# Performance work log

Measured on AMD Instinct MI355X. Metric: run time of the kernel, lower is better.

The kernel has to match this reference:

```python
import jax, jax.numpy as jnp
import numpy as np

B, T, U, QS, MS = 64, 2048, 512, 512, 512

def setup_inputs() -> dict:
    key = jax.random.key(0)
    k1, k2, k3, k4, k5 = jax.random.split(key, 5)
    query = jax.random.normal(k1, (B, QS), dtype=jnp.float32)
    keys = jax.random.normal(k2, (B, T, MS), dtype=jnp.float32)
    # torch nn.Linear weights: [out, in], no bias
    Wq = jax.random.normal(k3, (U, QS), dtype=jnp.float32) * (1.0 / np.sqrt(QS))
    Wm = jax.random.normal(k4, (U, MS), dtype=jnp.float32) * (1.0 / np.sqrt(MS))
    Wa = jax.random.normal(k5, (1, U), dtype=jnp.float32) * (1.0 / np.sqrt(U))
    return {"query": query, "keys": keys, "Wq": Wq, "Wm": Wm, "Wa": Wa}

def reference(query, keys, Wq, Wm, Wa):
    # processed_query: [B, U]
    pq = jnp.einsum('bq,uq->bu', query, Wq)
    # values: [B, T, U]
    vals = jnp.einsum('btm,um->btu', keys, Wm)
    # alignment score: [B, T]
    score = jnp.einsum('btu,u->bt', jnp.tanh(pq[:, None, :] + vals), Wa[0])
    weight = jax.nn.softmax(score, axis=-1)            # [B, T]
    total_context = jnp.einsum('bt,btm->bm', weight, keys)  # [B, MS]
    return (total_context, score)
```

## Files before the change

kernel.cpp:

```cpp
#include <hip/hip_runtime.h>
#include <cstdint>
#include <cstddef>

#define Bn 64
#define Tn 2048
#define Un 512
#define QSn 512
#define MSn 512
#define TCH 64
#define NCH 32
#define NKT 16

using f32x16 = __attribute__((ext_vector_type(16))) float;
using bf16x8 = __attribute__((ext_vector_type(8))) short;

__device__ __forceinline__ unsigned short f2bf(float x) {
    unsigned int u = __float_as_uint(x);
    u += 0x7FFFu + ((u >> 16) & 1u);
    return (unsigned short)(u >> 16);
}

__device__ __forceinline__ unsigned int pk2bf(float lo, float hi) {
    unsigned int r;
    asm("v_cvt_pk_bf16_f32 %0, %1, %2" : "=v"(r) : "v"(lo), "v"(hi));
    return r;
}

__device__ __forceinline__ bf16x8 cvt8(float4 a, float4 b) {
    union { unsigned int u[4]; bf16x8 v; } r;
    r.u[0] = pk2bf(a.x, a.y);
    r.u[1] = pk2bf(a.z, a.w);
    r.u[2] = pk2bf(b.x, b.y);
    r.u[3] = pk2bf(b.z, b.w);
    return r.v;
}

__device__ __forceinline__ float tanh_fast(float x) {
    float e = exp2f(x * 2.885390043258667f);
    return 1.f - 2.f * __builtin_amdgcn_rcpf(e + 1.f);
}

#define GLOAD(G, L) __builtin_amdgcn_global_load_lds( \
    (const __attribute__((address_space(1))) void*)(G), \
    (__attribute__((address_space(3))) void*)(L), 16, 0, 0)

__global__ __launch_bounds__(256) void cvt_kernel(const float* __restrict__ src,
                                                  unsigned short* __restrict__ dst) {
    int i = blockIdx.x * 256 + threadIdx.x;
    float4 v = *(const float4*)(src + (size_t)i * 4);
    ushort4 h = { f2bf(v.x), f2bf(v.y), f2bf(v.z), f2bf(v.w) };
    *(ushort4*)&dst[(size_t)i * 4] = h;
}

__global__ __launch_bounds__(128) void pq_kernel(const float* __restrict__ query,
                                                 const float* __restrict__ Wq,
                                                 float* __restrict__ pq) {
    __shared__ float ql[QSn];
    const int b = blockIdx.x;
    const int quad = blockIdx.y;
    const int tid = threadIdx.x;
    for (int i = tid; i < QSn; i += 128) ql[i] = query[(size_t)b * QSn + i];
    __syncthreads();
    const int u = quad * 128 + tid;
    const float* w = Wq + (size_t)u * QSn;
    float a0 = 0.f, a1 = 0.f;
    #pragma unroll 4
    for (int k = 0; k < QSn; k += 8) {
        float4 w0 = *(const float4*)(w + k);
        float4 w1 = *(const float4*)(w + k + 4);
        float4 q0 = *(const float4*)(ql + k);
        float4 q1 = *(const float4*)(ql + k + 4);
        a0 += w0.x * q0.x + w0.y * q0.y + w0.z * q0.z + w0.w * q0.w;
        a1 += w1.x * q1.x + w1.y * q1.y + w1.z * q1.z + w1.w * q1.w;
    }
    pq[(size_t)b * Un + u] = a0 + a1;
}

__global__ __launch_bounds__(512, 4) void fused_kernel(const float* __restrict__ keys,
                                                       const unsigned short* __restrict__ WmB,
                                                       const float* __restrict__ pq,
                                                       const float* __restrict__ Wa,
                                                       float* __restrict__ score_out,
                                                       float* __restrict__ pm,
                                                       float* __restrict__ pl,
                                                       float* __restrict__ pctx) {
    __shared__ __align__(16) unsigned short Ah[2][TCH * 32];
    __shared__ __align__(16) unsigned short Bh[2][512 * 32];
    __shared__ float sc_lds[8][TCH];
    __shared__ float stot[TCH];
    __shared__ float wexp[TCH];

    const int tid = threadIdx.x;
    const int lane = tid & 63;
    const int w = tid >> 6;
    const int lc = lane & 31;
    const int l5 = lane >> 5;
    const int b = blockIdx.y;
    const int chunk = blockIdx.x;
    const int t0 = chunk * TCH;

    const int ar = tid >> 2;
    const int akg = tid & 3;
    const int awof = (tid >> 3) * 64 +
                     ((((akg << 1) | (ar & 1)) ^ ((tid >> 3) & 7)) * 8);
    const float* gA = keys + ((size_t)b * Tn + t0 + ar) * MSn + akg * 8;

    const int bg = (lane & 7) ^ ((lane >> 3) & 7);
    const unsigned short* gBw = WmB +
        (size_t)(w * 64 + (((lane >> 3) << 1) | (bg & 1))) * MSn + (bg >> 1) * 8;

    f32x16 acc[2][2];
    #pragma unroll
    for (int mf = 0; mf < 2; ++mf)
        #pragma unroll
        for (int nf = 0; nf < 2; ++nf)
            #pragma unroll
            for (int r = 0; r < 16; ++r) acc[mf][nf][r] = 0.f;

    {
        char* bD = (char*)&Bh[0][0] + w * 4096;
        #pragma unroll
        for (int j = 0; j < 4; ++j)
            GLOAD(gBw + (size_t)j * 16 * MSn, bD + j * 1024);
        if (tid < 256) {
            float4 p0 = *(const float4*)(gA);
            float4 p1 = *(const float4*)(gA + 4);
            *(bf16x8*)&Ah[0][awof] = cvt8(p0, p1);
        }
    }

    #pragma unroll
    for (int kt = 0; kt < NKT; ++kt) {
        __syncthreads();

        float4 p0, p1;
        if (kt < NKT - 1 && tid < 256) {
            const float* g = gA + (kt + 1) * 32;
            p0 = *(const float4*)(g);
            p1 = *(const float4*)(g + 4);
        }

        {
            const unsigned short* lA = &Ah[kt & 1][0];
            const unsigned short* lB = &Bh[kt & 1][0];
            #pragma unroll
            for (int ks = 0; ks < 2; ++ks) {
                bf16x8 af[2], bfr[2];
                #pragma unroll
                for (int mf = 0; mf < 2; ++mf) {
                    int r = mf * 32 + lc;
                    int gp = (((ks * 2 + l5) << 1) | (r & 1)) ^ ((r >> 1) & 7);
                    af[mf] = *(const bf16x8*)&lA[(r >> 1) * 64 + gp * 8];
                }
                #pragma unroll
                for (int nf = 0; nf < 2; ++nf) {
                    int ru = w * 64 + nf * 32 + lc;
                    int gp = (((ks * 2 + l5) << 1) | (ru & 1)) ^ ((ru >> 1) & 7);
                    bfr[nf] = *(const bf16x8*)&Bh[kt & 1][(ru >> 1) * 64 + gp * 8];
                    (void)lB;
                }
                #pragma unroll
                for (int mf = 0; mf < 2; ++mf)
                    #pragma unroll
                    for (int nf = 0; nf < 2; ++nf)
                        acc[mf][nf] = __builtin_amdgcn_mfma_f32_32x32x16_bf16(
                            af[mf], bfr[nf], acc[mf][nf], 0, 0, 0);
            }
        }

        __syncthreads();

        if (kt < NKT - 1) {
            char* bD = (char*)&Bh[(kt + 1) & 1][0] + w * 4096;
            const unsigned short* gb = gBw + (kt + 1) * 32;
            #pragma unroll
            for (int j = 0; j < 4; ++j)
                GLOAD(gb + (size_t)j * 16 * MSn, bD + j * 1024);
            if (tid < 256)
                *(bf16x8*)&Ah[(kt + 1) & 1][awof] = cvt8(p0, p1);
        }
    }

    float pqv[2], wav[2];
    #pragma unroll
    for (int nf = 0; nf < 2; ++nf) {
        int u = w * 64 + nf * 32 + lc;
        pqv[nf] = pq[(size_t)b * Un + u];
        wav[nf] = Wa[u];
    }
    #pragma unroll
    for (int mf = 0; mf < 2; ++mf) {
        #pragma unroll
        for (int r = 0; r < 16; ++r) {
            float s = tanh_fast(acc[mf][0][r] + pqv[0]) * wav[0]
                    + tanh_fast(acc[mf][1][r] + pqv[1]) * wav[1];
            s += __shfl_xor(s, 16);
            s += __shfl_xor(s, 8);
            s += __shfl_xor(s, 4);
            s += __shfl_xor(s, 2);
            s += __shfl_xor(s, 1);
            if (lc == 0)
                sc_lds[w][mf * 32 + (r & 3) + 8 * (r >> 2) + 4 * l5] = s;
        }
    }
    __syncthreads();
    if (tid < TCH) {
        float v = ((sc_lds[0][tid] + sc_lds[1][tid]) + (sc_lds[2][tid] + sc_lds[3][tid]))
                + ((sc_lds[4][tid] + sc_lds[5][tid]) + (sc_lds[6][tid] + sc_lds[7][tid]));
        stot[tid] = v;
        score_out[(size_t)b * Tn + t0 + tid] = v;
    }
    __syncthreads();

    if (tid < 64) {
        float v = stot[tid];
        float mx = v;
        #pragma unroll
        for (int off = 32; off; off >>= 1) mx = fmaxf(mx, __shfl_xor(mx, off));
        float e = __expf(v - mx);
        wexp[tid] = e;
        float sum = e;
        #pragma unroll
        for (int off = 32; off; off >>= 1) sum += __shfl_xor(sum, off);
        if (tid == 0) {
            pm[b * NCH + chunk] = mx;
            pl[b * NCH + chunk] = sum;
        }
    }
    __syncthreads();

    const float* kp = keys + ((size_t)b * Tn + t0) * MSn + tid;
    float cx = 0.f;
    #pragma unroll 8
    for (int t = 0; t < TCH; ++t)
        cx += wexp[t] * kp[(size_t)t * MSn];
    pctx[((size_t)(b * NCH + chunk)) * MSn + tid] = cx;
}

__global__ __launch_bounds__(512) void merge_kernel(const float* __restrict__ pm,
                                                    const float* __restrict__ pl,
                                                    const float* __restrict__ pctx,
                                                    float* __restrict__ ctx) {
    __shared__ float sm[NCH], sl[NCH];
    const int b = blockIdx.x, tid = threadIdx.x;
    if (tid < NCH) {
        sm[tid] = pm[b * NCH + tid];
        sl[tid] = pl[b * NCH + tid];
    }
    __syncthreads();
    float M = -1e30f;
    #pragma unroll
    for (int c = 0; c < NCH; ++c) M = fmaxf(M, sm[c]);
    float L = 0.f;
    #pragma unroll
    for (int c = 0; c < NCH; ++c) L += sl[c] * __expf(sm[c] - M);
    const float inv = 1.f / L;
    float acc = 0.f;
    #pragma unroll
    for (int c = 0; c < NCH; ++c)
        acc += __expf(sm[c] - M) * pctx[((size_t)(b * NCH + c)) * MSn + tid];
    ctx[(size_t)b * MSn + tid] = acc * inv;
}

extern "C" void kernel_launch(void* const* d_in, const int* in_sizes, int n_in,
                              void* d_out, int out_size, void* d_ws, size_t ws_size,
                              hipStream_t stream) {
    const float* query = (const float*)d_in[0];
    const float* keys  = (const float*)d_in[1];
    const float* Wq    = (const float*)d_in[2];
    const float* Wm    = (const float*)d_in[3];
    const float* Wa    = (const float*)d_in[4];

    float* ctx_out   = (float*)d_out;
    float* score_out = (float*)d_out + (size_t)Bn * MSn;

    char* ws = (char*)d_ws;
    float* ws_pq   = (float*)(ws);
    unsigned short* ws_wmbf = (unsigned short*)(ws + 131072);
    float* ws_pm   = (float*)(ws + 655360);
    float* ws_pl   = (float*)(ws + 663552);
    float* ws_pctx = (float*)(ws + 671744);

    cvt_kernel<<<(Un * MSn / 4) / 256, 256, 0, stream>>>(Wm, ws_wmbf);
    pq_kernel<<<dim3(Bn, 4), 128, 0, stream>>>(query, Wq, ws_pq);
    fused_kernel<<<dim3(NCH, Bn), 512, 0, stream>>>(keys, ws_wmbf, ws_pq, Wa,
                                                    score_out, ws_pm, ws_pl, ws_pctx);
    merge_kernel<<<Bn, 512, 0, stream>>>(ws_pm, ws_pl, ws_pctx, ctx_out);
}
```

Baseline: 174.7 us.

## Restructure the GEMM k-loop pipeline to one barrier per step with explicit waitcnt

The k-loop now issues the next A-tile global load and B-tile LDS-direct loads before the barrier. It uses an explicit s_waitcnt vmcnt(5) so only the current tile is waited on, and drops the second __syncthreads per iteration. This is safe because each wave stages only its own B rows. The A tile load is spread across all threads with 4 floats each instead of half the threads loading 8. The pq/Wa loads are hoisted before the loop, and sched_barriers pin the instruction order. The intent is to cut barrier stalls and overlap memory with MFMA. The cost is reliance on hand-counted vmcnt values and compiler scheduling fences.

```diff
diff --git a/kernel.cpp b/kernel.cpp
--- a/kernel.cpp
+++ b/kernel.cpp
@@ -26,15 +26,6 @@
     return r;
 }
 
-__device__ __forceinline__ bf16x8 cvt8(float4 a, float4 b) {
-    union { unsigned int u[4]; bf16x8 v; } r;
-    r.u[0] = pk2bf(a.x, a.y);
-    r.u[1] = pk2bf(a.z, a.w);
-    r.u[2] = pk2bf(b.x, b.y);
-    r.u[3] = pk2bf(b.z, b.w);
-    return r.v;
-}
-
 __device__ __forceinline__ float tanh_fast(float x) {
     float e = exp2f(x * 2.885390043258667f);
     return 1.f - 2.f * __builtin_amdgcn_rcpf(e + 1.f);
@@ -43,6 +34,8 @@
 #define GLOAD(G, L) __builtin_amdgcn_global_load_lds( \
     (const __attribute__((address_space(1))) void*)(G), \
     (__attribute__((address_space(3))) void*)(L), 16, 0, 0)
+
+#define SB() __builtin_amdgcn_sched_barrier(0)
 
 __global__ __launch_bounds__(256) void cvt_kernel(const float* __restrict__ src,
                                                   unsigned short* __restrict__ dst) {
@@ -99,16 +92,25 @@
     const int chunk = blockIdx.x;
     const int t0 = chunk * TCH;
 
-    const int ar = tid >> 2;
-    const int akg = tid & 3;
-    const int awof = (tid >> 3) * 64 +
-                     ((((akg << 1) | (ar & 1)) ^ ((tid >> 3) & 7)) * 8);
-    const float* gA = keys + ((size_t)b * Tn + t0 + ar) * MSn + akg * 8;
+    const int ar = tid >> 3;
+    const int kq = tid & 7;
+    const int awof = (ar >> 1) * 64 +
+                     (((((kq >> 1) << 1) | (ar & 1)) ^ ((ar >> 1) & 7)) * 8) +
+                     (kq & 1) * 4;
+    const float* gA = keys + ((size_t)b * Tn + t0 + ar) * MSn + kq * 4;
 
     const int bg = (lane & 7) ^ ((lane >> 3) & 7);
     const unsigned short* gBw = WmB +
         (size_t)(w * 64 + (((lane >> 3) << 1) | (bg & 1))) * MSn + (bg >> 1) * 8;
 
+    #define STAGE_B(KT, BUF) do { \
+        const unsigned short* gb_ = gBw + (KT) * 32; \
+        char* bD_ = (char*)&Bh[BUF][0] + w * 4096; \
+        GLOAD(gb_,                    bD_); \
+        GLOAD(gb_ + (size_t)16 * MSn, bD_ + 1024); \
+        GLOAD(gb_ + (size_t)32 * MSn, bD_ + 2048); \
+        GLOAD(gb_ + (size_t)48 * MSn, bD_ + 3072); } while (0)
+
     f32x16 acc[2][2];
     #pragma unroll
     for (int mf = 0; mf < 2; ++mf)
@@ -117,28 +119,39 @@
             #pragma unroll
             for (int r = 0; r < 16; ++r) acc[mf][nf][r] = 0.f;
 
+    float pqv[2], wav[2];
+    #pragma unroll
+    for (int nf = 0; nf < 2; ++nf) {
+        int u = w * 64 + nf * 32 + lc;
+        pqv[nf] = pq[(size_t)b * Un + u];
+        wav[nf] = Wa[u];
+    }
+    SB();
     {
-        char* bD = (char*)&Bh[0][0] + w * 4096;
-        #pragma unroll
-        for (int j = 0; j < 4; ++j)
-            GLOAD(gBw + (size_t)j * 16 * MSn, bD + j * 1024);
-        if (tid < 256) {
-            float4 p0 = *(const float4*)(gA);
-            float4 p1 = *(const float4*)(gA + 4);
-            *(bf16x8*)&Ah[0][awof] = cvt8(p0, p1);
-        }
+        float4 p = *(const float4*)(gA);
+        SB();
+        STAGE_B(0, 0);
+        SB();
+        uint2 h;
+        h.x = pk2bf(p.x, p.y);
+        h.y = pk2bf(p.z, p.w);
+        *(uint2*)&Ah[0][awof] = h;
     }
 
     #pragma unroll
     for (int kt = 0; kt < NKT; ++kt) {
-        __syncthreads();
-
-        float4 p0, p1;
-        if (kt < NKT - 1 && tid < 256) {
-            const float* g = gA + (kt + 1) * 32;
-            p0 = *(const float4*)(g);
-            p1 = *(const float4*)(g + 4);
-        }
+        float4 p;
+        if (kt < NKT - 1) {
+            p = *(const float4*)(gA + (kt + 1) * 32);
+            SB();
+            STAGE_B(kt + 1, (kt + 1) & 1);
+            SB();
+            asm volatile("s_waitcnt vmcnt(5) lgkmcnt(0)" ::: "memory");
+        } else {
+            asm volatile("s_waitcnt vmcnt(0) lgkmcnt(0)" ::: "memory");
+        }
+        __builtin_amdgcn_s_barrier();
+        SB();
 
         {
             const unsigned short* lA = &Ah[kt & 1][0];
@@ -156,8 +169,7 @@
                 for (int nf = 0; nf < 2; ++nf) {
                     int ru = w * 64 + nf * 32 + lc;
                     int gp = (((ks * 2 + l5) << 1) | (ru & 1)) ^ ((ru >> 1) & 7);
-                    bfr[nf] = *(const bf16x8*)&Bh[kt & 1][(ru >> 1) * 64 + gp * 8];
-                    (void)lB;
+                    bfr[nf] = *(const bf16x8*)&lB[(ru >> 1) * 64 + gp * 8];
                 }
                 #pragma unroll
                 for (int mf = 0; mf < 2; ++mf)
@@ -167,27 +179,17 @@
                             af[mf], bfr[nf], acc[mf][nf], 0, 0, 0);
             }
         }
-
-        __syncthreads();
+        SB();
 
         if (kt < NKT - 1) {
-            char* bD = (char*)&Bh[(kt + 1) & 1][0] + w * 4096;
-            const unsigned short* gb = gBw + (kt + 1) * 32;
-            #pragma unroll
-            for (int j = 0; j < 4; ++j)
-                GLOAD(gb + (size_t)j * 16 * MSn, bD + j * 1024);
-            if (tid < 256)
-                *(bf16x8*)&Ah[(kt + 1) & 1][awof] = cvt8(p0, p1);
-        }
-    }
-
-    float pqv[2], wav[2];
-    #pragma unroll
-    for (int nf = 0; nf < 2; ++nf) {
-        int u = w * 64 + nf * 32 + lc;
-        pqv[nf] = pq[(size_t)b * Un + u];
-        wav[nf] = Wa[u];
-    }
+            uint2 h;
+            h.x = pk2bf(p.x, p.y);
+            h.y = pk2bf(p.z, p.w);
+            *(uint2*)&Ah[(kt + 1) & 1][awof] = h;
+        }
+    }
+    #undef STAGE_B
+
     #pragma unroll
     for (int mf = 0; mf < 2; ++mf) {
         #pragma unroll
```

After: 167.9 us. 3.9% less time.
